# Optimization experiments

Hardware: AMD Instinct MI355X
Metric: run time of the kernel (lower is better)

Reference implementation:

```python
import jax, jax.numpy as jnp
import numpy as np

NUM_EXPERTS = 64
TOP_K = 2

def setup_inputs() -> dict:
    key = jax.random.key(0)
    k1, k2, k3, k4 = jax.random.split(key, 4)
    B, N, C, E = 4, 4096, 2048, NUM_EXPERTS
    x = jax.random.normal(k1, (B, N, C), dtype=jnp.float32)
    routing_context = jax.random.normal(k2, (B, C), dtype=jnp.float32)
    # Linear(C, E, bias=False) and Linear(C, C, bias=False), torch layout (out, in)
    gate_w = jax.random.normal(k3, (E, C), dtype=jnp.float32) * (1.0 / np.sqrt(C))
    ctx_w = jax.random.normal(k4, (C, C), dtype=jnp.float32) * (1.0 / np.sqrt(C))
    return {"x": x, "routing_context": routing_context, "gate_w": gate_w, "ctx_w": ctx_w}

def reference(x, routing_context, gate_w, ctx_w):
    B, N, C = x.shape
    T = B * N
    E = gate_w.shape[0]
    # context_proj(routing_context): (B,C) @ (C,C)^T -> broadcast over N
    ctx = routing_context @ ctx_w.T                      # (B, C)
    x_routing = (x + ctx[:, None, :]).reshape(T, C)      # (T, C)
    logits = x_routing @ gate_w.T                        # (T, E)
    top_vals, top_idx = jax.lax.top_k(logits, TOP_K)     # (T, K) each
    top_weights = jax.nn.softmax(top_vals, axis=-1)      # (T, K)
    probs = jax.nn.softmax(logits, axis=-1)              # (T, E)
    importance = probs.sum(axis=0) / T                   # (E,)
    # load: fraction of tokens that pick each expert in their top-k
    load = jnp.zeros((E,), dtype=probs.dtype).at[top_idx.reshape(-1)].add(1.0) / T
    aux_loss = E * (importance * load).sum()
    return top_idx, top_weights, aux_loss
```

## Files before the change

kernel.cpp:

```cpp
#include <hip/hip_runtime.h>
#include <math.h>

#define T_TOKENS 16384
#define C_DIM    2048
#define N_SEQ    4096
#define E_EXP    64
#define NSLICE   4
#define KSLICE   512
#define EPB      1024
#define GN       131072

typedef __attribute__((ext_vector_type(8))) short  short8;
typedef __attribute__((ext_vector_type(4))) float  floatx4;

__device__ __forceinline__ void splitv(float v, ushort& h, ushort& m, ushort& l) {
    unsigned u = __float_as_uint(v);
    h = (ushort)(u >> 16);
    float f1 = v - __uint_as_float(u & 0xffff0000u);
    unsigned u1 = __float_as_uint(f1);
    m = (ushort)(u1 >> 16);
    float f2 = f1 - __uint_as_float(u1 & 0xffff0000u);
    l = (ushort)(__float_as_uint(f2) >> 16);
}

__device__ __forceinline__ void splitpack8(const float4& a, const float4& b,
                                           short8& h, short8& m, short8& l) {
    ushort hh, mm, ll;
    splitv(a.x, hh, mm, ll); h[0] = hh; m[0] = mm; l[0] = ll;
    splitv(a.y, hh, mm, ll); h[1] = hh; m[1] = mm; l[1] = ll;
    splitv(a.z, hh, mm, ll); h[2] = hh; m[2] = mm; l[2] = ll;
    splitv(a.w, hh, mm, ll); h[3] = hh; m[3] = mm; l[3] = ll;
    splitv(b.x, hh, mm, ll); h[4] = hh; m[4] = mm; l[4] = ll;
    splitv(b.y, hh, mm, ll); h[5] = hh; m[5] = mm; l[5] = ll;
    splitv(b.z, hh, mm, ll); h[6] = hh; m[6] = mm; l[6] = ll;
    splitv(b.w, hh, mm, ll); h[7] = hh; m[7] = mm; l[7] = ll;
}

__device__ __forceinline__ void split3rne(float v, ushort& h, ushort& m, ushort& l) {
    unsigned u = __float_as_uint(v);
    unsigned r = (u + 0x7fffu + ((u >> 16) & 1u)) >> 16;
    h = (ushort)r;
    float e1 = v - __uint_as_float(r << 16);
    u = __float_as_uint(e1);
    r = (u + 0x7fffu + ((u >> 16) & 1u)) >> 16;
    m = (ushort)r;
    float e2 = e1 - __uint_as_float(r << 16);
    l = (ushort)(__float_as_uint(e2) >> 16);
}

__global__ __launch_bounds__(256, 2) void pre_kernel(
    const float* __restrict__ rc, const float* __restrict__ ctx_w,
    const float* __restrict__ gw, float* __restrict__ ctx_out,
    ushort* __restrict__ gsp)
{
    if (gsp != nullptr) {
        const int idx  = blockIdx.x * 256 + threadIdx.x;
        const int j    = idx & 7;
        const int e    = (idx >> 3) & 63;
        const int koct = idx >> 9;
        float g = gw[(size_t)e * C_DIM + koct * 8 + j];
        ushort h, m, l;
        split3rne(g, h, m, l);
        gsp[idx]          = h;
        gsp[GN + idx]     = m;
        gsp[2 * GN + idx] = l;
    }

    const int w    = threadIdx.x >> 6;
    const int lane = threadIdx.x & 63;
    const int j    = blockIdx.x * 4 + w;

    const float4* wr = (const float4*)(ctx_w + (size_t)j * C_DIM);
    const float4* r0 = (const float4*)(rc);
    const float4* r1 = (const float4*)(rc + C_DIM);
    const float4* r2 = (const float4*)(rc + 2 * C_DIM);
    const float4* r3 = (const float4*)(rc + 3 * C_DIM);

    float s0 = 0.f, s1 = 0.f, s2 = 0.f, s3 = 0.f;
#pragma unroll
    for (int it = 0; it < 8; ++it) {
        float4 a  = wr[it * 64 + lane];
        float4 c0 = r0[it * 64 + lane];
        float4 c1 = r1[it * 64 + lane];
        float4 c2 = r2[it * 64 + lane];
        float4 c3 = r3[it * 64 + lane];
        s0 += a.x * c0.x + a.y * c0.y + a.z * c0.z + a.w * c0.w;
        s1 += a.x * c1.x + a.y * c1.y + a.z * c1.z + a.w * c1.w;
        s2 += a.x * c2.x + a.y * c2.y + a.z * c2.z + a.w * c2.w;
        s3 += a.x * c3.x + a.y * c3.y + a.z * c3.z + a.w * c3.w;
    }
#pragma unroll
    for (int off = 32; off; off >>= 1) {
        s0 += __shfl_xor(s0, off, 64);
        s1 += __shfl_xor(s1, off, 64);
        s2 += __shfl_xor(s2, off, 64);
        s3 += __shfl_xor(s3, off, 64);
    }
    if (lane == 0) {
        ctx_out[j]             = s0;
        ctx_out[C_DIM + j]     = s1;
        ctx_out[2 * C_DIM + j] = s2;
        ctx_out[3 * C_DIM + j] = s3;
    }
}

__global__ __launch_bounds__(256, 2) void gemm_cl_kernel(
    const float* __restrict__ x, const ushort* __restrict__ gsp,
    const float* __restrict__ gw, const float* __restrict__ ctx,
    float* __restrict__ P, float* __restrict__ cl)
{
    if (blockIdx.x >= 128 * NSLICE) {
        const int lane = threadIdx.x & 63;
        const int pk   = (blockIdx.x - 128 * NSLICE) * 4 + (threadIdx.x >> 6);
        const int b    = pk >> 6;
        const int e    = pk & 63;
        const float4* wr = (const float4*)(gw + (size_t)e * C_DIM);
        const float4* cr = (const float4*)(ctx + (size_t)b * C_DIM);
        float s = 0.f;
#pragma unroll
        for (int it = 0; it < 8; ++it) {
            float4 a = wr[it * 64 + lane];
            float4 c = cr[it * 64 + lane];
            s += a.x * c.x + a.y * c.y + a.z * c.z + a.w * c.w;
        }
#pragma unroll
        for (int off = 32; off; off >>= 1) s += __shfl_xor(s, off, 64);
        if (lane == 0) cl[pk] = s;
        return;
    }

    const int tid   = threadIdx.x;
    const int wv    = tid >> 6;
    const int lane  = tid & 63;
    const int l15   = lane & 15;
    const int quad  = lane >> 4;
    const int tile  = blockIdx.x & 127;
    const int slice = blockIdx.x >> 7;
    const int tw    = tile * 128 + wv * 32;
    const int cbase = slice * KSLICE;

    floatx4 acc[2][4];
#pragma unroll
    for (int s = 0; s < 2; ++s)
#pragma unroll
        for (int nt = 0; nt < 4; ++nt) acc[s][nt] = (floatx4){0.f, 0.f, 0.f, 0.f};

    const float* xr0 = x + (size_t)(tw + l15) * C_DIM + cbase + quad * 8;
    const float* xr1 = xr0 + (size_t)16 * C_DIM;
    const ushort* bb = gsp + ((size_t)((cbase >> 3) + quad) * 64 + l15) * 8;

    const int NKS = KSLICE / 32;

    float4 a00 = *(const float4*)(xr0);
    float4 a01 = *(const float4*)(xr0 + 4);
    float4 a10 = *(const float4*)(xr1);
    float4 a11 = *(const float4*)(xr1 + 4);

#pragma unroll 2
    for (int ks = 0; ks < NKS; ++ks) {
        const int nk = (ks + 1 < NKS) ? (ks + 1) : 0;
        float4 n00 = *(const float4*)(xr0 + nk * 32);
        float4 n01 = *(const float4*)(xr0 + nk * 32 + 4);
        float4 n10 = *(const float4*)(xr1 + nk * 32);
        float4 n11 = *(const float4*)(xr1 + nk * 32 + 4);

        const ushort* bks = bb + (size_t)ks * 4 * 64 * 8;
        short8 bh[4], bm[4], bl[4];
#pragma unroll
        for (int nt = 0; nt < 4; ++nt) {
            const ushort* bp_ = bks + (size_t)(16 * nt) * 8;
            bh[nt] = *(const short8*)(bp_);
            bm[nt] = *(const short8*)(bp_ + GN);
            bl[nt] = *(const short8*)(bp_ + 2 * (size_t)GN);
        }

        short8 ah0, am0, al0, ah1, am1, al1;
        splitpack8(a00, a01, ah0, am0, al0);
        splitpack8(a10, a11, ah1, am1, al1);

#pragma unroll
        for (int nt = 0; nt < 4; ++nt) {
            acc[0][nt] = __builtin_amdgcn_mfma_f32_16x16x32_bf16(ah0, bh[nt], acc[0][nt], 0, 0, 0);
            acc[0][nt] = __builtin_amdgcn_mfma_f32_16x16x32_bf16(ah0, bm[nt], acc[0][nt], 0, 0, 0);
            acc[0][nt] = __builtin_amdgcn_mfma_f32_16x16x32_bf16(am0, bh[nt], acc[0][nt], 0, 0, 0);
            acc[0][nt] = __builtin_amdgcn_mfma_f32_16x16x32_bf16(ah0, bl[nt], acc[0][nt], 0, 0, 0);
            acc[0][nt] = __builtin_amdgcn_mfma_f32_16x16x32_bf16(al0, bh[nt], acc[0][nt], 0, 0, 0);
            acc[0][nt] = __builtin_amdgcn_mfma_f32_16x16x32_bf16(am0, bm[nt], acc[0][nt], 0, 0, 0);
            acc[1][nt] = __builtin_amdgcn_mfma_f32_16x16x32_bf16(ah1, bh[nt], acc[1][nt], 0, 0, 0);
            acc[1][nt] = __builtin_amdgcn_mfma_f32_16x16x32_bf16(ah1, bm[nt], acc[1][nt], 0, 0, 0);
            acc[1][nt] = __builtin_amdgcn_mfma_f32_16x16x32_bf16(am1, bh[nt], acc[1][nt], 0, 0, 0);
            acc[1][nt] = __builtin_amdgcn_mfma_f32_16x16x32_bf16(ah1, bl[nt], acc[1][nt], 0, 0, 0);
            acc[1][nt] = __builtin_amdgcn_mfma_f32_16x16x32_bf16(al1, bh[nt], acc[1][nt], 0, 0, 0);
            acc[1][nt] = __builtin_amdgcn_mfma_f32_16x16x32_bf16(am1, bm[nt], acc[1][nt], 0, 0, 0);
        }

        a00 = n00; a01 = n01; a10 = n10; a11 = n11;
    }

    float* Ps = P + ((size_t)slice * T_TOKENS + tw) * E_EXP;
#pragma unroll
    for (int s = 0; s < 2; ++s)
#pragma unroll
        for (int nt = 0; nt < 4; ++nt)
#pragma unroll
            for (int r = 0; r < 4; ++r)
                Ps[(size_t)(s * 16 + quad * 4 + r) * E_EXP + 16 * nt + l15] =
                    acc[s][nt][r];
}

__global__ __launch_bounds__(256) void epilogue_kernel(
    const float* __restrict__ P, const float* __restrict__ cl,
    float* __restrict__ out, float* __restrict__ bp)
{
    __shared__ float red[4][128];

    const int tid  = threadIdx.x;
    const int wv   = tid >> 6;
    const int lane = tid & 63;
    const int t0   = blockIdx.x * (T_TOKENS / EPB);
    const float clv = cl[(t0 >> 12) * 64 + lane];

    float imp_acc = 0.f, cnt_acc = 0.f;

    for (int tt = 0; tt < 4; ++tt) {
        const int t = t0 + wv * 4 + tt;
        float v = clv;
#pragma unroll
        for (int s = 0; s < NSLICE; ++s)
            v += P[((size_t)s * T_TOKENS + t) * E_EXP + lane];

        const float p = expf(v);
        float v1 = v;  int i1 = lane;
        float v2 = -INFINITY; int i2 = 0x7fffffff;
        float s = p;
#pragma unroll
        for (int off = 32; off; off >>= 1) {
            float ov1 = __shfl_xor(v1, off, 64);
            int   oi1 = __shfl_xor(i1, off, 64);
            float ov2 = __shfl_xor(v2, off, 64);
            int   oi2 = __shfl_xor(i2, off, 64);
            s += __shfl_xor(s, off, 64);
            const bool aw = (ov1 < v1) || (ov1 == v1 && i1 < oi1);
            const float lv = aw ? ov1 : v1;  const int li = aw ? oi1 : i1;
            const float wv2 = aw ? v2 : ov2; const int wi = aw ? i2 : oi2;
            if (!aw) { v1 = ov1; i1 = oi1; }
            const bool sw = (wv2 < lv) || (wv2 == lv && li < wi);
            v2 = sw ? lv : wv2; i2 = sw ? li : wi;
        }

        imp_acc += p / s;
        if (lane == i1 || lane == i2) cnt_acc += 1.f;

        if (lane == 0) {
            const float e2 = expf(v2 - v1);
            out[2 * t]     = (float)i1;
            out[2 * t + 1] = (float)i2;
            out[2 * T_TOKENS + 2 * t]     = 1.f / (1.f + e2);
            out[2 * T_TOKENS + 2 * t + 1] = e2 / (1.f + e2);
        }
    }

    red[wv][lane]      = imp_acc;
    red[wv][64 + lane] = cnt_acc;
    __syncthreads();
    if (tid < 128) {
        float s = red[0][tid] + red[1][tid] + red[2][tid] + red[3][tid];
        bp[(size_t)blockIdx.x * 128 + tid] = s;
    }
}

__global__ __launch_bounds__(1024) void aux_kernel(
    const float* __restrict__ bp, int nb, float* __restrict__ out_aux)
{
    __shared__ float4 red[32][32];
    const int tid = threadIdx.x;
    const int c4  = tid & 31;
    const int grp = tid >> 5;

    const float4* bp4 = (const float4*)bp;
    float4 s = make_float4(0.f, 0.f, 0.f, 0.f);
    for (int r = grp; r < nb; r += 32) {
        float4 v = bp4[(size_t)r * 32 + c4];
        s.x += v.x; s.y += v.y; s.z += v.z; s.w += v.w;
    }
    red[grp][c4] = s;
    __syncthreads();

    if (tid < 32) {
        float4 t = make_float4(0.f, 0.f, 0.f, 0.f);
#pragma unroll
        for (int g = 0; g < 32; ++g) {
            float4 v = red[g][tid];
            t.x += v.x; t.y += v.y; t.z += v.z; t.w += v.w;
        }
        red[0][tid] = t;
    }
    __syncthreads();

    if (tid < 16) {
        float4 a = red[0][tid];
        float4 b = red[0][tid + 16];
        float v = a.x * b.x + a.y * b.y + a.z * b.z + a.w * b.w;
#pragma unroll
        for (int off = 8; off; off >>= 1) v += __shfl_xor(v, off, 64);
        if (tid == 0)
            out_aux[0] = (float)E_EXP * v / ((float)T_TOKENS * (float)T_TOKENS);
    }
}

#define TM    64
#define FKC   64
#define FLSTR 68
__global__ __launch_bounds__(256) void router_fused_kernel(
    const float* __restrict__ x, const float* __restrict__ gate_w,
    const float* __restrict__ ctx, float* __restrict__ out,
    float* __restrict__ bp)
{
    __shared__ float xs[TM][FLSTR];
    __shared__ float gs[E_EXP][FLSTR];
    __shared__ float ls[TM][FLSTR];
    __shared__ float red[4][128];

    const int tid = threadIdx.x;
    const int eg  = tid & 15;
    const int tg  = tid >> 4;
    const int t0  = blockIdx.x * TM;
    const int b   = t0 / N_SEQ;
    const int sr  = tid >> 4;
    const int scg = tid & 15;
    const float* ctx_row = ctx + (size_t)b * C_DIM;

    float4 acc[4][4];
#pragma unroll
    for (int i = 0; i < 4; ++i)
#pragma unroll
        for (int j = 0; j < 4; ++j) acc[i][j] = make_float4(0.f, 0.f, 0.f, 0.f);

    float4 px[4], pg[4], pc;
    auto prefetch = [&](int kc) {
        const int c0 = kc * FKC + scg * 4;
        pc = *(const float4*)(ctx_row + c0);
#pragma unroll
        for (int i = 0; i < 4; ++i) {
            px[i] = *(const float4*)(x + (size_t)(t0 + sr + 16 * i) * C_DIM + c0);
            pg[i] = *(const float4*)(gate_w + (size_t)(sr + 16 * i) * C_DIM + c0);
        }
    };

    prefetch(0);
    const int NCHUNK = C_DIM / FKC;
    for (int kc = 0; kc < NCHUNK; ++kc) {
        __syncthreads();
#pragma unroll
        for (int i = 0; i < 4; ++i) {
            float4 v = px[i];
            v.x += pc.x; v.y += pc.y; v.z += pc.z; v.w += pc.w;
            *(float4*)&xs[sr + 16 * i][scg * 4] = v;
            *(float4*)&gs[sr + 16 * i][scg * 4] = pg[i];
        }
        __syncthreads();
        if (kc + 1 < NCHUNK) prefetch(kc + 1);
#pragma unroll
        for (int cc = 0; cc < FKC; cc += 4) {
            float4 xv[4], gv[4];
#pragma unroll
            for (int i = 0; i < 4; ++i) xv[i] = *(const float4*)&xs[tg + 16 * i][cc];
#pragma unroll
            for (int j = 0; j < 4; ++j) gv[j] = *(const float4*)&gs[eg + 16 * j][cc];
#pragma unroll
            for (int i = 0; i < 4; ++i)
#pragma unroll
                for (int j = 0; j < 4; ++j) {
                    acc[i][j].x = fmaf(xv[i].x, gv[j].x, acc[i][j].x);
                    acc[i][j].y = fmaf(xv[i].y, gv[j].y, acc[i][j].y);
                    acc[i][j].z = fmaf(xv[i].z, gv[j].z, acc[i][j].z);
                    acc[i][j].w = fmaf(xv[i].w, gv[j].w, acc[i][j].w);
                }
        }
    }

    __syncthreads();
#pragma unroll
    for (int i = 0; i < 4; ++i)
#pragma unroll
        for (int j = 0; j < 4; ++j)
            ls[tg + 16 * i][eg + 16 * j] =
                (acc[i][j].x + acc[i][j].y) + (acc[i][j].z + acc[i][j].w);
    __syncthreads();

    const int wv   = tid >> 6;
    const int lane = tid & 63;
    float imp_acc = 0.f, cnt_acc = 0.f;

    for (int tt = 0; tt < 16; ++tt) {
        const int tokL = wv * 16 + tt;
        const float v = ls[tokL][lane];
        const float p = expf(v);
        float v1 = v;  int i1 = lane;
        float v2 = -INFINITY; int i2 = 0x7fffffff;
        float s = p;
#pragma unroll
        for (int off = 32; off; off >>= 1) {
            float ov1 = __shfl_xor(v1, off, 64);
            int   oi1 = __shfl_xor(i1, off, 64);
            float ov2 = __shfl_xor(v2, off, 64);
            int   oi2 = __shfl_xor(i2, off, 64);
            s += __shfl_xor(s, off, 64);
            const bool aw = (ov1 < v1) || (ov1 == v1 && i1 < oi1);
            const float lv = aw ? ov1 : v1;  const int li = aw ? oi1 : i1;
            const float wv2 = aw ? v2 : ov2; const int wi = aw ? i2 : oi2;
            if (!aw) { v1 = ov1; i1 = oi1; }
            const bool sw = (wv2 < lv) || (wv2 == lv && li < wi);
            v2 = sw ? lv : wv2; i2 = sw ? li : wi;
        }
        imp_acc += p / s;
        if (lane == i1 || lane == i2) cnt_acc += 1.f;
        if (lane == 0) {
            const int t = t0 + tokL;
            const float e2 = expf(v2 - v1);
            out[2 * t]     = (float)i1;
            out[2 * t + 1] = (float)i2;
            out[2 * T_TOKENS + 2 * t]     = 1.f / (1.f + e2);
            out[2 * T_TOKENS + 2 * t + 1] = e2 / (1.f + e2);
        }
    }

    red[wv][lane]      = imp_acc;
    red[wv][64 + lane] = cnt_acc;
    __syncthreads();
    if (tid < 128) {
        float s = red[0][tid] + red[1][tid] + red[2][tid] + red[3][tid];
        bp[(size_t)blockIdx.x * 128 + tid] = s;
    }
}

extern "C" void kernel_launch(void* const* d_in, const int* in_sizes, int n_in,
                              void* d_out, int out_size, void* d_ws, size_t ws_size,
                              hipStream_t stream)
{
    (void)in_sizes; (void)n_in; (void)out_size;
    const float* x      = (const float*)d_in[0];
    const float* rc     = (const float*)d_in[1];
    const float* gate_w = (const float*)d_in[2];
    const float* ctx_w  = (const float*)d_in[3];
    float* out = (float*)d_out;

    float*  ctx = (float*)d_ws;
    float*  cl  = ctx + 8192;
    float*  bp  = cl + 256;
    float*  P   = bp + (size_t)EPB * 128;
    ushort* gsp = (ushort*)(P + (size_t)NSLICE * T_TOKENS * E_EXP);

    const size_t need =
        (8192 + 256 + (size_t)EPB * 128 + (size_t)NSLICE * T_TOKENS * E_EXP)
            * sizeof(float)
        + (size_t)3 * GN * sizeof(ushort);

    if (ws_size >= need) {
        pre_kernel<<<512, 256, 0, stream>>>(rc, ctx_w, gate_w, ctx, gsp);
        gemm_cl_kernel<<<128 * NSLICE + 64, 256, 0, stream>>>(x, gsp, gate_w, ctx, P, cl);
        epilogue_kernel<<<EPB, 256, 0, stream>>>(P, cl, out, bp);
        aux_kernel<<<1, 1024, 0, stream>>>(bp, EPB, out + 2 * 2 * T_TOKENS);
    } else {
        pre_kernel<<<512, 256, 0, stream>>>(rc, ctx_w, gate_w, ctx, nullptr);
        router_fused_kernel<<<256, 256, 0, stream>>>(x, gate_w, ctx, out, bp);
        aux_kernel<<<1, 1024, 0, stream>>>(bp, 256, out + 2 * 2 * T_TOKENS);
    }
}
```

Baseline: 246.2 us.

## Overlap context projection with the main GEMM and move cl into its own kernel

The context-projection GEMV (ctx_w @ routing_context) moves out of the pre-kernel and into extra blocks of the main bf16-split GEMM kernel, so its 16 MB ctx_w read runs alongside the x GEMM. The pre-stage now only does the gate weight split. The ctx-by-gate_w dot products (cl) go into a small separate kernel launched after the GEMM, because they depend on ctx. This adds one kernel launch, and the extra ctx blocks compete with the GEMM tiles for bandwidth and compute units.

```diff
diff --git a/kernel.cpp b/kernel.cpp
--- a/kernel.cpp
+++ b/kernel.cpp
@@ -48,28 +48,10 @@
     l = (ushort)(__float_as_uint(e2) >> 16);
 }
 
-__global__ __launch_bounds__(256, 2) void pre_kernel(
-    const float* __restrict__ rc, const float* __restrict__ ctx_w,
-    const float* __restrict__ gw, float* __restrict__ ctx_out,
-    ushort* __restrict__ gsp)
-{
-    if (gsp != nullptr) {
-        const int idx  = blockIdx.x * 256 + threadIdx.x;
-        const int j    = idx & 7;
-        const int e    = (idx >> 3) & 63;
-        const int koct = idx >> 9;
-        float g = gw[(size_t)e * C_DIM + koct * 8 + j];
-        ushort h, m, l;
-        split3rne(g, h, m, l);
-        gsp[idx]          = h;
-        gsp[GN + idx]     = m;
-        gsp[2 * GN + idx] = l;
-    }
-
-    const int w    = threadIdx.x >> 6;
-    const int lane = threadIdx.x & 63;
-    const int j    = blockIdx.x * 4 + w;
-
+__device__ __forceinline__ void ctx_body(
+    int j, int lane, const float* __restrict__ rc,
+    const float* __restrict__ ctx_w, float* __restrict__ ctx_out)
+{
     const float4* wr = (const float4*)(ctx_w + (size_t)j * C_DIM);
     const float4* r0 = (const float4*)(rc);
     const float4* r1 = (const float4*)(rc + C_DIM);
@@ -104,28 +86,30 @@
     }
 }
 
-__global__ __launch_bounds__(256, 2) void gemm_cl_kernel(
+__global__ __launch_bounds__(256) void split_kernel(
+    const float* __restrict__ gw, ushort* __restrict__ gsp)
+{
+    const int idx  = blockIdx.x * 256 + threadIdx.x;
+    const int j    = idx & 7;
+    const int e    = (idx >> 3) & 63;
+    const int koct = idx >> 9;
+    float g = gw[(size_t)e * C_DIM + koct * 8 + j];
+    ushort h, m, l;
+    split3rne(g, h, m, l);
+    gsp[idx]          = h;
+    gsp[GN + idx]     = m;
+    gsp[2 * GN + idx] = l;
+}
+
+__global__ __launch_bounds__(256, 2) void gemm_ctx_kernel(
     const float* __restrict__ x, const ushort* __restrict__ gsp,
-    const float* __restrict__ gw, const float* __restrict__ ctx,
-    float* __restrict__ P, float* __restrict__ cl)
+    const float* __restrict__ rc, const float* __restrict__ ctx_w,
+    float* __restrict__ ctx_out, float* __restrict__ P)
 {
     if (blockIdx.x >= 128 * NSLICE) {
         const int lane = threadIdx.x & 63;
-        const int pk   = (blockIdx.x - 128 * NSLICE) * 4 + (threadIdx.x >> 6);
-        const int b    = pk >> 6;
-        const int e    = pk & 63;
-        const float4* wr = (const float4*)(gw + (size_t)e * C_DIM);
-        const float4* cr = (const float4*)(ctx + (size_t)b * C_DIM);
-        float s = 0.f;
-#pragma unroll
-        for (int it = 0; it < 8; ++it) {
-            float4 a = wr[it * 64 + lane];
-            float4 c = cr[it * 64 + lane];
-            s += a.x * c.x + a.y * c.y + a.z * c.z + a.w * c.w;
-        }
-#pragma unroll
-        for (int off = 32; off; off >>= 1) s += __shfl_xor(s, off, 64);
-        if (lane == 0) cl[pk] = s;
+        const int j = (blockIdx.x - 128 * NSLICE) * 4 + (threadIdx.x >> 6);
+        ctx_body(j, lane, rc, ctx_w, ctx_out);
         return;
     }
 
@@ -208,6 +192,28 @@
                     acc[s][nt][r];
 }
 
+__global__ __launch_bounds__(256) void cl_kernel(
+    const float* __restrict__ gw, const float* __restrict__ ctx,
+    float* __restrict__ cl)
+{
+    const int lane = threadIdx.x & 63;
+    const int pk   = blockIdx.x * 4 + (threadIdx.x >> 6);
+    const int b    = pk >> 6;
+    const int e    = pk & 63;
+    const float4* wr = (const float4*)(gw + (size_t)e * C_DIM);
+    const float4* cr = (const float4*)(ctx + (size_t)b * C_DIM);
+    float s = 0.f;
+#pragma unroll
+    for (int it = 0; it < 8; ++it) {
+        float4 a = wr[it * 64 + lane];
+        float4 c = cr[it * 64 + lane];
+        s += a.x * c.x + a.y * c.y + a.z * c.z + a.w * c.w;
+    }
+#pragma unroll
+    for (int off = 32; off; off >>= 1) s += __shfl_xor(s, off, 64);
+    if (lane == 0) cl[pk] = s;
+}
+
 __global__ __launch_bounds__(256) void epilogue_kernel(
     const float* __restrict__ P, const float* __restrict__ cl,
     float* __restrict__ out, float* __restrict__ bp)
@@ -308,6 +314,15 @@
     }
 }
 
+__global__ __launch_bounds__(256) void ctx_only_kernel(
+    const float* __restrict__ rc, const float* __restrict__ ctx_w,
+    float* __restrict__ ctx_out)
+{
+    const int lane = threadIdx.x & 63;
+    const int j    = blockIdx.x * 4 + (threadIdx.x >> 6);
+    ctx_body(j, lane, rc, ctx_w, ctx_out);
+}
+
 #define TM    64
 #define FKC   64
 #define FLSTR 68
@@ -457,12 +472,14 @@
         + (size_t)3 * GN * sizeof(ushort);
 
     if (ws_size >= need) {
-        pre_kernel<<<512, 256, 0, stream>>>(rc, ctx_w, gate_w, ctx, gsp);
-        gemm_cl_kernel<<<128 * NSLICE + 64, 256, 0, stream>>>(x, gsp, gate_w, ctx, P, cl);
+        split_kernel<<<512, 256, 0, stream>>>(gate_w, gsp);
+        gemm_ctx_kernel<<<128 * NSLICE + 512, 256, 0, stream>>>(
+            x, gsp, rc, ctx_w, ctx, P);
+        cl_kernel<<<64, 256, 0, stream>>>(gate_w, ctx, cl);
         epilogue_kernel<<<EPB, 256, 0, stream>>>(P, cl, out, bp);
         aux_kernel<<<1, 1024, 0, stream>>>(bp, EPB, out + 2 * 2 * T_TOKENS);
     } else {
-        pre_kernel<<<512, 256, 0, stream>>>(rc, ctx_w, gate_w, ctx, nullptr);
+        ctx_only_kernel<<<512, 256, 0, stream>>>(rc, ctx_w, ctx);
         router_fused_kernel<<<256, 256, 0, stream>>>(x, gate_w, ctx, out, bp);
         aux_kernel<<<1, 1024, 0, stream>>>(bp, 256, out + 2 * 2 * T_TOKENS);
     }
```

New measurement: 245.8 us. Within noise of the previous version (-0.1%).

## Fuse full-K MFMA gate GEMM with top-k epilogue, drop split-K partials

Applied to the files above, without the earlier changes.

Replaces the split-K GEMM plus separate epilogue with one kernel where each 2-wave block computes full-K logits for 32 tokens and does top-2, softmax and per-block reductions in registers via lane shuffles. This eliminates writing and rereading the 4-slice partial logit buffer and one kernel launch. The context-logit bias moves to a small standalone kernel. The tradeoff is fewer, longer-running waves with lower occupancy, which may reduce latency hiding on the dominant x stream.

```diff
diff --git a/kernel.cpp b/kernel.cpp
--- a/kernel.cpp
+++ b/kernel.cpp
@@ -5,10 +5,8 @@
 #define C_DIM    2048
 #define N_SEQ    4096
 #define E_EXP    64
-#define NSLICE   4
-#define KSLICE   512
-#define EPB      1024
 #define GN       131072
+#define FBLK     512
 
 typedef __attribute__((ext_vector_type(8))) short  short8;
 typedef __attribute__((ext_vector_type(4))) float  floatx4;
@@ -48,7 +46,45 @@
     l = (ushort)(__float_as_uint(e2) >> 16);
 }
 
-__global__ __launch_bounds__(256, 2) void pre_kernel(
+__device__ __forceinline__ void ctx_body(
+    int j, int lane, const float* __restrict__ rc,
+    const float* __restrict__ ctx_w, float* __restrict__ ctx_out)
+{
+    const float4* wr = (const float4*)(ctx_w + (size_t)j * C_DIM);
+    const float4* r0 = (const float4*)(rc);
+    const float4* r1 = (const float4*)(rc + C_DIM);
+    const float4* r2 = (const float4*)(rc + 2 * C_DIM);
+    const float4* r3 = (const float4*)(rc + 3 * C_DIM);
+
+    float s0 = 0.f, s1 = 0.f, s2 = 0.f, s3 = 0.f;
+#pragma unroll
+    for (int it = 0; it < 8; ++it) {
+        float4 a  = wr[it * 64 + lane];
+        float4 c0 = r0[it * 64 + lane];
+        float4 c1 = r1[it * 64 + lane];
+        float4 c2 = r2[it * 64 + lane];
+        float4 c3 = r3[it * 64 + lane];
+        s0 += a.x * c0.x + a.y * c0.y + a.z * c0.z + a.w * c0.w;
+        s1 += a.x * c1.x + a.y * c1.y + a.z * c1.z + a.w * c1.w;
+        s2 += a.x * c2.x + a.y * c2.y + a.z * c2.z + a.w * c2.w;
+        s3 += a.x * c3.x + a.y * c3.y + a.z * c3.z + a.w * c3.w;
+    }
+#pragma unroll
+    for (int off = 32; off; off >>= 1) {
+        s0 += __shfl_xor(s0, off, 64);
+        s1 += __shfl_xor(s1, off, 64);
+        s2 += __shfl_xor(s2, off, 64);
+        s3 += __shfl_xor(s3, off, 64);
+    }
+    if (lane == 0) {
+        ctx_out[j]             = s0;
+        ctx_out[C_DIM + j]     = s1;
+        ctx_out[2 * C_DIM + j] = s2;
+        ctx_out[3 * C_DIM + j] = s3;
+    }
+}
+
+__global__ __launch_bounds__(256) void pre_kernel(
     const float* __restrict__ rc, const float* __restrict__ ctx_w,
     const float* __restrict__ gw, float* __restrict__ ctx_out,
     ushort* __restrict__ gsp)
@@ -65,106 +101,66 @@
         gsp[GN + idx]     = m;
         gsp[2 * GN + idx] = l;
     }
-
-    const int w    = threadIdx.x >> 6;
     const int lane = threadIdx.x & 63;
-    const int j    = blockIdx.x * 4 + w;
-
-    const float4* wr = (const float4*)(ctx_w + (size_t)j * C_DIM);
-    const float4* r0 = (const float4*)(rc);
-    const float4* r1 = (const float4*)(rc + C_DIM);
-    const float4* r2 = (const float4*)(rc + 2 * C_DIM);
-    const float4* r3 = (const float4*)(rc + 3 * C_DIM);
-
-    float s0 = 0.f, s1 = 0.f, s2 = 0.f, s3 = 0.f;
+    const int j    = blockIdx.x * 4 + (threadIdx.x >> 6);
+    ctx_body(j, lane, rc, ctx_w, ctx_out);
+}
+
+__global__ __launch_bounds__(256) void cl_kernel(
+    const float* __restrict__ gw, const float* __restrict__ ctx,
+    float* __restrict__ cl)
+{
+    const int lane = threadIdx.x & 63;
+    const int pk   = blockIdx.x * 4 + (threadIdx.x >> 6);
+    const int b    = pk >> 6;
+    const int e    = pk & 63;
+    const float4* wr = (const float4*)(gw + (size_t)e * C_DIM);
+    const float4* cr = (const float4*)(ctx + (size_t)b * C_DIM);
+    float s = 0.f;
 #pragma unroll
     for (int it = 0; it < 8; ++it) {
-        float4 a  = wr[it * 64 + lane];
-        float4 c0 = r0[it * 64 + lane];
-        float4 c1 = r1[it * 64 + lane];
-        float4 c2 = r2[it * 64 + lane];
-        float4 c3 = r3[it * 64 + lane];
-        s0 += a.x * c0.x + a.y * c0.y + a.z * c0.z + a.w * c0.w;
-        s1 += a.x * c1.x + a.y * c1.y + a.z * c1.z + a.w * c1.w;
-        s2 += a.x * c2.x + a.y * c2.y + a.z * c2.z + a.w * c2.w;
-        s3 += a.x * c3.x + a.y * c3.y + a.z * c3.z + a.w * c3.w;
-    }
-#pragma unroll
-    for (int off = 32; off; off >>= 1) {
-        s0 += __shfl_xor(s0, off, 64);
-        s1 += __shfl_xor(s1, off, 64);
-        s2 += __shfl_xor(s2, off, 64);
-        s3 += __shfl_xor(s3, off, 64);
-    }
-    if (lane == 0) {
-        ctx_out[j]             = s0;
-        ctx_out[C_DIM + j]     = s1;
-        ctx_out[2 * C_DIM + j] = s2;
-        ctx_out[3 * C_DIM + j] = s3;
-    }
-}
-
-__global__ __launch_bounds__(256, 2) void gemm_cl_kernel(
+        float4 a = wr[it * 64 + lane];
+        float4 c = cr[it * 64 + lane];
+        s += a.x * c.x + a.y * c.y + a.z * c.z + a.w * c.w;
+    }
+#pragma unroll
+    for (int off = 32; off; off >>= 1) s += __shfl_xor(s, off, 64);
+    if (lane == 0) cl[pk] = s;
+}
+
+__global__ __launch_bounds__(128, 1) void fused_kernel(
     const float* __restrict__ x, const ushort* __restrict__ gsp,
-    const float* __restrict__ gw, const float* __restrict__ ctx,
-    float* __restrict__ P, float* __restrict__ cl)
-{
-    if (blockIdx.x >= 128 * NSLICE) {
-        const int lane = threadIdx.x & 63;
-        const int pk   = (blockIdx.x - 128 * NSLICE) * 4 + (threadIdx.x >> 6);
-        const int b    = pk >> 6;
-        const int e    = pk & 63;
-        const float4* wr = (const float4*)(gw + (size_t)e * C_DIM);
-        const float4* cr = (const float4*)(ctx + (size_t)b * C_DIM);
-        float s = 0.f;
-#pragma unroll
-        for (int it = 0; it < 8; ++it) {
-            float4 a = wr[it * 64 + lane];
-            float4 c = cr[it * 64 + lane];
-            s += a.x * c.x + a.y * c.y + a.z * c.z + a.w * c.w;
-        }
-#pragma unroll
-        for (int off = 32; off; off >>= 1) s += __shfl_xor(s, off, 64);
-        if (lane == 0) cl[pk] = s;
-        return;
-    }
-
-    const int tid   = threadIdx.x;
-    const int wv    = tid >> 6;
-    const int lane  = tid & 63;
-    const int l15   = lane & 15;
-    const int quad  = lane >> 4;
-    const int tile  = blockIdx.x & 127;
-    const int slice = blockIdx.x >> 7;
-    const int tw    = tile * 128 + wv * 32;
-    const int cbase = slice * KSLICE;
-
-    floatx4 acc[2][4];
-#pragma unroll
-    for (int s = 0; s < 2; ++s)
-#pragma unroll
-        for (int nt = 0; nt < 4; ++nt) acc[s][nt] = (floatx4){0.f, 0.f, 0.f, 0.f};
-
-    const float* xr0 = x + (size_t)(tw + l15) * C_DIM + cbase + quad * 8;
-    const float* xr1 = xr0 + (size_t)16 * C_DIM;
-    const ushort* bb = gsp + ((size_t)((cbase >> 3) + quad) * 64 + l15) * 8;
-
-    const int NKS = KSLICE / 32;
-
-    float4 a00 = *(const float4*)(xr0);
-    float4 a01 = *(const float4*)(xr0 + 4);
-    float4 a10 = *(const float4*)(xr1);
-    float4 a11 = *(const float4*)(xr1 + 4);
+    const float* __restrict__ cl, float* __restrict__ out,
+    float* __restrict__ bp)
+{
+    __shared__ float red[2][128];
+
+    const int tid  = threadIdx.x;
+    const int wv   = tid >> 6;
+    const int lane = tid & 63;
+    const int l15  = lane & 15;
+    const int quad = lane >> 4;
+    const int t0   = blockIdx.x * 32;
+    const int b    = t0 >> 12;
+
+    floatx4 acc[4];
+#pragma unroll
+    for (int nt = 0; nt < 4; ++nt) acc[nt] = (floatx4){0.f, 0.f, 0.f, 0.f};
+
+    const float* xr = x + (size_t)(t0 + wv * 16 + l15) * C_DIM + quad * 8;
+
+    float4 a00 = *(const float4*)(xr);
+    float4 a01 = *(const float4*)(xr + 4);
+    float4 n00 = *(const float4*)(xr + 32);
+    float4 n01 = *(const float4*)(xr + 36);
 
 #pragma unroll 2
-    for (int ks = 0; ks < NKS; ++ks) {
-        const int nk = (ks + 1 < NKS) ? (ks + 1) : 0;
-        float4 n00 = *(const float4*)(xr0 + nk * 32);
-        float4 n01 = *(const float4*)(xr0 + nk * 32 + 4);
-        float4 n10 = *(const float4*)(xr1 + nk * 32);
-        float4 n11 = *(const float4*)(xr1 + nk * 32 + 4);
-
-        const ushort* bks = bb + (size_t)ks * 4 * 64 * 8;
+    for (int ks = 0; ks < 64; ++ks) {
+        const int fk = (ks + 2 < 64) ? ks + 2 : 0;
+        float4 f00 = *(const float4*)(xr + fk * 32);
+        float4 f01 = *(const float4*)(xr + fk * 32 + 4);
+
+        const ushort* bks = gsp + ((size_t)(ks * 4 + quad) * 64 + l15) * 8;
         short8 bh[4], bm[4], bl[4];
 #pragma unroll
         for (int nt = 0; nt < 4; ++nt) {
@@ -174,61 +170,225 @@
             bl[nt] = *(const short8*)(bp_ + 2 * (size_t)GN);
         }
 
-        short8 ah0, am0, al0, ah1, am1, al1;
-        splitpack8(a00, a01, ah0, am0, al0);
-        splitpack8(a10, a11, ah1, am1, al1);
+        short8 ah, am, al;
+        splitpack8(a00, a01, ah, am, al);
 
 #pragma unroll
         for (int nt = 0; nt < 4; ++nt) {
-            acc[0][nt] = __builtin_amdgcn_mfma_f32_16x16x32_bf16(ah0, bh[nt], acc[0][nt], 0, 0, 0);
-            acc[0][nt] = __builtin_amdgcn_mfma_f32_16x16x32_bf16(ah0, bm[nt], acc[0][nt], 0, 0, 0);
-            acc[0][nt] = __builtin_amdgcn_mfma_f32_16x16x32_bf16(am0, bh[nt], acc[0][nt], 0, 0, 0);
-            acc[0][nt] = __builtin_amdgcn_mfma_f32_16x16x32_bf16(ah0, bl[nt], acc[0][nt], 0, 0, 0);
-            acc[0][nt] = __builtin_amdgcn_mfma_f32_16x16x32_bf16(al0, bh[nt], acc[0][nt], 0, 0, 0);
-            acc[0][nt] = __builtin_amdgcn_mfma_f32_16x16x32_bf16(am0, bm[nt], acc[0][nt], 0, 0, 0);
-            acc[1][nt] = __builtin_amdgcn_mfma_f32_16x16x32_bf16(ah1, bh[nt], acc[1][nt], 0, 0, 0);
-            acc[1][nt] = __builtin_amdgcn_mfma_f32_16x16x32_bf16(ah1, bm[nt], acc[1][nt], 0, 0, 0);
-            acc[1][nt] = __builtin_amdgcn_mfma_f32_16x16x32_bf16(am1, bh[nt], acc[1][nt], 0, 0, 0);
-            acc[1][nt] = __builtin_amdgcn_mfma_f32_16x16x32_bf16(ah1, bl[nt], acc[1][nt], 0, 0, 0);
-            acc[1][nt] = __builtin_amdgcn_mfma_f32_16x16x32_bf16(al1, bh[nt], acc[1][nt], 0, 0, 0);
-            acc[1][nt] = __builtin_amdgcn_mfma_f32_16x16x32_bf16(am1, bm[nt], acc[1][nt], 0, 0, 0);
-        }
-
-        a00 = n00; a01 = n01; a10 = n10; a11 = n11;
-    }
-
-    float* Ps = P + ((size_t)slice * T_TOKENS + tw) * E_EXP;
-#pragma unroll
-    for (int s = 0; s < 2; ++s)
-#pragma unroll
-        for (int nt = 0; nt < 4; ++nt)
-#pragma unroll
-            for (int r = 0; r < 4; ++r)
-                Ps[(size_t)(s * 16 + quad * 4 + r) * E_EXP + 16 * nt + l15] =
-                    acc[s][nt][r];
-}
-
-__global__ __launch_bounds__(256) void epilogue_kernel(
-    const float* __restrict__ P, const float* __restrict__ cl,
-    float* __restrict__ out, float* __restrict__ bp)
-{
+            acc[nt] = __builtin_amdgcn_mfma_f32_16x16x32_bf16(ah, bh[nt], acc[nt], 0, 0, 0);
+            acc[nt] = __builtin_amdgcn_mfma_f32_16x16x32_bf16(ah, bm[nt], acc[nt], 0, 0, 0);
+            acc[nt] = __builtin_amdgcn_mfma_f32_16x16x32_bf16(am, bh[nt], acc[nt], 0, 0, 0);
+            acc[nt] = __builtin_amdgcn_mfma_f32_16x16x32_bf16(ah, bl[nt], acc[nt], 0, 0, 0);
+            acc[nt] = __builtin_amdgcn_mfma_f32_16x16x32_bf16(al, bh[nt], acc[nt], 0, 0, 0);
+            acc[nt] = __builtin_amdgcn_mfma_f32_16x16x32_bf16(am, bm[nt], acc[nt], 0, 0, 0);
+        }
+
+        a00 = n00; a01 = n01; n00 = f00; n01 = f01;
+    }
+
+    float clv[4];
+#pragma unroll
+    for (int nt = 0; nt < 4; ++nt) clv[nt] = cl[b * 64 + 16 * nt + l15];
+
+    float imp4[4] = {0.f, 0.f, 0.f, 0.f};
+    float cnt4[4] = {0.f, 0.f, 0.f, 0.f};
+
+#pragma unroll
+    for (int r = 0; r < 4; ++r) {
+        const int t = t0 + wv * 16 + quad * 4 + r;
+        float v[4], p[4];
+#pragma unroll
+        for (int nt = 0; nt < 4; ++nt) {
+            v[nt] = acc[nt][r] + clv[nt];
+            p[nt] = expf(v[nt]);
+        }
+        float s = (p[0] + p[1]) + (p[2] + p[3]);
+
+        float v1 = v[0];      int i1 = l15;
+        float v2 = -INFINITY; int i2 = 0x7fffffff;
+#pragma unroll
+        for (int k = 1; k < 4; ++k) {
+            const int e = 16 * k + l15;
+            if (v[k] > v1) { v2 = v1; i2 = i1; v1 = v[k]; i1 = e; }
+            else if (v[k] > v2 || (v[k] == v2 && e < i2)) { v2 = v[k]; i2 = e; }
+        }
+
+#pragma unroll
+        for (int off = 8; off; off >>= 1) {
+            float ov1 = __shfl_xor(v1, off, 64);
+            int   oi1 = __shfl_xor(i1, off, 64);
+            float ov2 = __shfl_xor(v2, off, 64);
+            int   oi2 = __shfl_xor(i2, off, 64);
+            s += __shfl_xor(s, off, 64);
+            const bool aw = (ov1 < v1) || (ov1 == v1 && i1 < oi1);
+            const float lv = aw ? ov1 : v1;  const int li = aw ? oi1 : i1;
+            const float wv2 = aw ? v2 : ov2; const int wi = aw ? i2 : oi2;
+            if (!aw) { v1 = ov1; i1 = oi1; }
+            const bool sw = (wv2 < lv) || (wv2 == lv && li < wi);
+            v2 = sw ? lv : wv2; i2 = sw ? li : wi;
+        }
+
+#pragma unroll
+        for (int nt = 0; nt < 4; ++nt) {
+            const int e = 16 * nt + l15;
+            imp4[nt] += p[nt] / s;
+            cnt4[nt] += ((e == i1) ? 1.f : 0.f) + ((e == i2) ? 1.f : 0.f);
+        }
+
+        if (l15 == 0) {
+            const float e2 = expf(v2 - v1);
+            out[2 * t]     = (float)i1;
+            out[2 * t + 1] = (float)i2;
+            out[2 * T_TOKENS + 2 * t]     = 1.f / (1.f + e2);
+            out[2 * T_TOKENS + 2 * t + 1] = e2 / (1.f + e2);
+        }
+    }
+
+#pragma unroll
+    for (int nt = 0; nt < 4; ++nt) {
+        imp4[nt] += __shfl_xor(imp4[nt], 16, 64);
+        imp4[nt] += __shfl_xor(imp4[nt], 32, 64);
+        cnt4[nt] += __shfl_xor(cnt4[nt], 16, 64);
+        cnt4[nt] += __shfl_xor(cnt4[nt], 32, 64);
+    }
+    if (quad == 0) {
+#pragma unroll
+        for (int nt = 0; nt < 4; ++nt) {
+            red[wv][16 * nt + l15]      = imp4[nt];
+            red[wv][64 + 16 * nt + l15] = cnt4[nt];
+        }
+    }
+    __syncthreads();
+    if (tid < 128)
+        bp[(size_t)blockIdx.x * 128 + tid] = red[0][tid] + red[1][tid];
+}
+
+__global__ __launch_bounds__(1024) void aux_kernel(
+    const float* __restrict__ bp, int nb, float* __restrict__ out_aux)
+{
+    __shared__ float4 red[32][32];
+    const int tid = threadIdx.x;
+    const int c4  = tid & 31;
+    const int grp = tid >> 5;
+
+    const float4* bp4 = (const float4*)bp;
+    float4 s = make_float4(0.f, 0.f, 0.f, 0.f);
+    for (int r = grp; r < nb; r += 32) {
+        float4 v = bp4[(size_t)r * 32 + c4];
+        s.x += v.x; s.y += v.y; s.z += v.z; s.w += v.w;
+    }
+    red[grp][c4] = s;
+    __syncthreads();
+
+    if (tid < 32) {
+        float4 t = make_float4(0.f, 0.f, 0.f, 0.f);
+#pragma unroll
+        for (int g = 0; g < 32; ++g) {
+            float4 v = red[g][tid];
+            t.x += v.x; t.y += v.y; t.z += v.z; t.w += v.w;
+        }
+        red[0][tid] = t;
+    }
+    __syncthreads();
+
+    if (tid < 16) {
+        float4 a = red[0][tid];
+        float4 b = red[0][tid + 16];
+        float v = a.x * b.x + a.y * b.y + a.z * b.z + a.w * b.w;
+#pragma unroll
+        for (int off = 8; off; off >>= 1) v += __shfl_xor(v, off, 64);
+        if (tid == 0)
+            out_aux[0] = (float)E_EXP * v / ((float)T_TOKENS * (float)T_TOKENS);
+    }
+}
+
+#define TM    64
+#define FKC   64
+#define FLSTR 68
+__global__ __launch_bounds__(256) void router_fused_kernel(
+    const float* __restrict__ x, const float* __restrict__ gate_w,
+    const float* __restrict__ ctx, float* __restrict__ out,
+    float* __restrict__ bp)
+{
+    __shared__ float xs[TM][FLSTR];
+    __shared__ float gs[E_EXP][FLSTR];
+    __shared__ float ls[TM][FLSTR];
     __shared__ float red[4][128];
 
-    const int tid  = threadIdx.x;
+    const int tid = threadIdx.x;
+    const int eg  = tid & 15;
+    const int tg  = tid >> 4;
+    const int t0  = blockIdx.x * TM;
+    const int b   = t0 / N_SEQ;
+    const int sr  = tid >> 4;
+    const int scg = tid & 15;
+    const float* ctx_row = ctx + (size_t)b * C_DIM;
+
+    float4 acc[4][4];
+#pragma unroll
+    for (int i = 0; i < 4; ++i)
+#pragma unroll
+        for (int j = 0; j < 4; ++j) acc[i][j] = make_float4(0.f, 0.f, 0.f, 0.f);
+
+    float4 px[4], pg[4], pc;
+    auto prefetch = [&](int kc) {
+        const int c0 = kc * FKC + scg * 4;
+        pc = *(const float4*)(ctx_row + c0);
+#pragma unroll
+        for (int i = 0; i < 4; ++i) {
+            px[i] = *(const float4*)(x + (size_t)(t0 + sr + 16 * i) * C_DIM + c0);
+            pg[i] = *(const float4*)(gate_w + (size_t)(sr + 16 * i) * C_DIM + c0);
+        }
+    };
+
+    prefetch(0);
+    const int NCHUNK = C_DIM / FKC;
+    for (int kc = 0; kc < NCHUNK; ++kc) {
+        __syncthreads();
+#pragma unroll
+        for (int i = 0; i < 4; ++i) {
+            float4 v = px[i];
+            v.x += pc.x; v.y += pc.y; v.z += pc.z; v.w += pc.w;
+            *(float4*)&xs[sr + 16 * i][scg * 4] = v;
+            *(float4*)&gs[sr + 16 * i][scg * 4] = pg[i];
+        }
+        __syncthreads();
+        if (kc + 1 < NCHUNK) prefetch(kc + 1);
+#pragma unroll
+        for (int cc = 0; cc < FKC; cc += 4) {
+            float4 xv[4], gv[4];
+#pragma unroll
+            for (int i = 0; i < 4; ++i) xv[i] = *(const float4*)&xs[tg + 16 * i][cc];
+#pragma unroll
+            for (int j = 0; j < 4; ++j) gv[j] = *(const float4*)&gs[eg + 16 * j][cc];
+#pragma unroll
+            for (int i = 0; i < 4; ++i)
+#pragma unroll
+                for (int j = 0; j < 4; ++j) {
+                    acc[i][j].x = fmaf(xv[i].x, gv[j].x, acc[i][j].x);
+                    acc[i][j].y = fmaf(xv[i].y, gv[j].y, acc[i][j].y);
+                    acc[i][j].z = fmaf(xv[i].z, gv[j].z, acc[i][j].z);
+                    acc[i][j].w = fmaf(xv[i].w, gv[j].w, acc[i][j].w);
+                }
+        }
+    }
+
+    __syncthreads();
+#pragma unroll
+    for (int i = 0; i < 4; ++i)
+#pragma unroll
+        for (int j = 0; j < 4; ++j)
+            ls[tg + 16 * i][eg + 16 * j] =
+                (acc[i][j].x + acc[i][j].y) + (acc[i][j].z + acc[i][j].w);
+    __syncthreads();
+
     const int wv   = tid >> 6;
     const int lane = tid & 63;
-    const int t0   = blockIdx.x * (T_TOKENS / EPB);
-    const float clv = cl[(t0 >> 12) * 64 + lane];
-
     float imp_acc = 0.f, cnt_acc = 0.f;
 
-    for (int tt = 0; tt < 4; ++tt) {
-        const int t = t0 + wv * 4 + tt;
-        float v = clv;
-#pragma unroll
-        for (int s = 0; s < NSLICE; ++s)
-            v += P[((size_t)s * T_TOKENS + t) * E_EXP + lane];
-
+    for (int tt = 0; tt < 16; ++tt) {
+        const int tokL = wv * 16 + tt;
+        const float v = ls[tokL][lane];
         const float p = expf(v);
         float v1 = v;  int i1 = lane;
         float v2 = -INFINITY; int i2 = 0x7fffffff;
@@ -247,172 +407,6 @@
             const bool sw = (wv2 < lv) || (wv2 == lv && li < wi);
             v2 = sw ? lv : wv2; i2 = sw ? li : wi;
         }
-
-        imp_acc += p / s;
-        if (lane == i1 || lane == i2) cnt_acc += 1.f;
-
-        if (lane == 0) {
-            const float e2 = expf(v2 - v1);
-            out[2 * t]     = (float)i1;
-            out[2 * t + 1] = (float)i2;
-            out[2 * T_TOKENS + 2 * t]     = 1.f / (1.f + e2);
-            out[2 * T_TOKENS + 2 * t + 1] = e2 / (1.f + e2);
-        }
-    }
-
-    red[wv][lane]      = imp_acc;
-    red[wv][64 + lane] = cnt_acc;
-    __syncthreads();
-    if (tid < 128) {
-        float s = red[0][tid] + red[1][tid] + red[2][tid] + red[3][tid];
-        bp[(size_t)blockIdx.x * 128 + tid] = s;
-    }
-}
-
-__global__ __launch_bounds__(1024) void aux_kernel(
-    const float* __restrict__ bp, int nb, float* __restrict__ out_aux)
-{
-    __shared__ float4 red[32][32];
-    const int tid = threadIdx.x;
-    const int c4  = tid & 31;
-    const int grp = tid >> 5;
-
-    const float4* bp4 = (const float4*)bp;
-    float4 s = make_float4(0.f, 0.f, 0.f, 0.f);
-    for (int r = grp; r < nb; r += 32) {
-        float4 v = bp4[(size_t)r * 32 + c4];
-        s.x += v.x; s.y += v.y; s.z += v.z; s.w += v.w;
-    }
-    red[grp][c4] = s;
-    __syncthreads();
-
-    if (tid < 32) {
-        float4 t = make_float4(0.f, 0.f, 0.f, 0.f);
-#pragma unroll
-        for (int g = 0; g < 32; ++g) {
-            float4 v = red[g][tid];
-            t.x += v.x; t.y += v.y; t.z += v.z; t.w += v.w;
-        }
-        red[0][tid] = t;
-    }
-    __syncthreads();
-
-    if (tid < 16) {
-        float4 a = red[0][tid];
-        float4 b = red[0][tid + 16];
-        float v = a.x * b.x + a.y * b.y + a.z * b.z + a.w * b.w;
-#pragma unroll
-        for (int off = 8; off; off >>= 1) v += __shfl_xor(v, off, 64);
-        if (tid == 0)
-            out_aux[0] = (float)E_EXP * v / ((float)T_TOKENS * (float)T_TOKENS);
-    }
-}
-
-#define TM    64
-#define FKC   64
-#define FLSTR 68
-__global__ __launch_bounds__(256) void router_fused_kernel(
-    const float* __restrict__ x, const float* __restrict__ gate_w,
-    const float* __restrict__ ctx, float* __restrict__ out,
-    float* __restrict__ bp)
-{
-    __shared__ float xs[TM][FLSTR];
-    __shared__ float gs[E_EXP][FLSTR];
-    __shared__ float ls[TM][FLSTR];
-    __shared__ float red[4][128];
-
-    const int tid = threadIdx.x;
-    const int eg  = tid & 15;
-    const int tg  = tid >> 4;
-    const int t0  = blockIdx.x * TM;
-    const int b   = t0 / N_SEQ;
-    const int sr  = tid >> 4;
-    const int scg = tid & 15;
-    const float* ctx_row = ctx + (size_t)b * C_DIM;
-
-    float4 acc[4][4];
-#pragma unroll
-    for (int i = 0; i < 4; ++i)
-#pragma unroll
-        for (int j = 0; j < 4; ++j) acc[i][j] = make_float4(0.f, 0.f, 0.f, 0.f);
-
-    float4 px[4], pg[4], pc;
-    auto prefetch = [&](int kc) {
-        const int c0 = kc * FKC + scg * 4;
-        pc = *(const float4*)(ctx_row + c0);
-#pragma unroll
-        for (int i = 0; i < 4; ++i) {
-            px[i] = *(const float4*)(x + (size_t)(t0 + sr + 16 * i) * C_DIM + c0);
-            pg[i] = *(const float4*)(gate_w + (size_t)(sr + 16 * i) * C_DIM + c0);
-        }
-    };
-
-    prefetch(0);
-    const int NCHUNK = C_DIM / FKC;
-    for (int kc = 0; kc < NCHUNK; ++kc) {
-        __syncthreads();
-#pragma unroll
-        for (int i = 0; i < 4; ++i) {
-            float4 v = px[i];
-            v.x += pc.x; v.y += pc.y; v.z += pc.z; v.w += pc.w;
-            *(float4*)&xs[sr + 16 * i][scg * 4] = v;
-            *(float4*)&gs[sr + 16 * i][scg * 4] = pg[i];
-        }
-        __syncthreads();
-        if (kc + 1 < NCHUNK) prefetch(kc + 1);
-#pragma unroll
-        for (int cc = 0; cc < FKC; cc += 4) {
-            float4 xv[4], gv[4];
-#pragma unroll
-            for (int i = 0; i < 4; ++i) xv[i] = *(const float4*)&xs[tg + 16 * i][cc];
-#pragma unroll
-            for (int j = 0; j < 4; ++j) gv[j] = *(const float4*)&gs[eg + 16 * j][cc];
-#pragma unroll
-            for (int i = 0; i < 4; ++i)
-#pragma unroll
-                for (int j = 0; j < 4; ++j) {
-                    acc[i][j].x = fmaf(xv[i].x, gv[j].x, acc[i][j].x);
-                    acc[i][j].y = fmaf(xv[i].y, gv[j].y, acc[i][j].y);
-                    acc[i][j].z = fmaf(xv[i].z, gv[j].z, acc[i][j].z);
-                    acc[i][j].w = fmaf(xv[i].w, gv[j].w, acc[i][j].w);
-                }
-        }
-    }
-
-    __syncthreads();
-#pragma unroll
-    for (int i = 0; i < 4; ++i)
-#pragma unroll
-        for (int j = 0; j < 4; ++j)
-            ls[tg + 16 * i][eg + 16 * j] =
-                (acc[i][j].x + acc[i][j].y) + (acc[i][j].z + acc[i][j].w);
-    __syncthreads();
-
-    const int wv   = tid >> 6;
-    const int lane = tid & 63;
-    float imp_acc = 0.f, cnt_acc = 0.f;
-
-    for (int tt = 0; tt < 16; ++tt) {
-        const int tokL = wv * 16 + tt;
-        const float v = ls[tokL][lane];
-        const float p = expf(v);
-        float v1 = v;  int i1 = lane;
-        float v2 = -INFINITY; int i2 = 0x7fffffff;
-        float s = p;
-#pragma unroll
-        for (int off = 32; off; off >>= 1) {
-            float ov1 = __shfl_xor(v1, off, 64);
-            int   oi1 = __shfl_xor(i1, off, 64);
-            float ov2 = __shfl_xor(v2, off, 64);
-            int   oi2 = __shfl_xor(i2, off, 64);
-            s += __shfl_xor(s, off, 64);
-            const bool aw = (ov1 < v1) || (ov1 == v1 && i1 < oi1);
-            const float lv = aw ? ov1 : v1;  const int li = aw ? oi1 : i1;
-            const float wv2 = aw ? v2 : ov2; const int wi = aw ? i2 : oi2;
-            if (!aw) { v1 = ov1; i1 = oi1; }
-            const bool sw = (wv2 < lv) || (wv2 == lv && li < wi);
-            v2 = sw ? lv : wv2; i2 = sw ? li : wi;
-        }
         imp_acc += p / s;
         if (lane == i1 || lane == i2) cnt_acc += 1.f;
         if (lane == 0) {
@@ -448,19 +442,17 @@
     float*  ctx = (float*)d_ws;
     float*  cl  = ctx + 8192;
     float*  bp  = cl + 256;
-    float*  P   = bp + (size_t)EPB * 128;
-    ushort* gsp = (ushort*)(P + (size_t)NSLICE * T_TOKENS * E_EXP);
+    ushort* gsp = (ushort*)(bp + (size_t)FBLK * 128);
 
     const size_t need =
-        (8192 + 256 + (size_t)EPB * 128 + (size_t)NSLICE * T_TOKENS * E_EXP)
-            * sizeof(float)
+        (8192 + 256 + (size_t)FBLK * 128) * sizeof(float)
         + (size_t)3 * GN * sizeof(ushort);
 
     if (ws_size >= need) {
         pre_kernel<<<512, 256, 0, stream>>>(rc, ctx_w, gate_w, ctx, gsp);
-        gemm_cl_kernel<<<128 * NSLICE + 64, 256, 0, stream>>>(x, gsp, gate_w, ctx, P, cl);
-        epilogue_kernel<<<EPB, 256, 0, stream>>>(P, cl, out, bp);
-        aux_kernel<<<1, 1024, 0, stream>>>(bp, EPB, out + 2 * 2 * T_TOKENS);
+        cl_kernel<<<64, 256, 0, stream>>>(gate_w, ctx, cl);
+        fused_kernel<<<FBLK, 128, 0, stream>>>(x, gsp, cl, out, bp);
+        aux_kernel<<<1, 1024, 0, stream>>>(bp, FBLK, out + 2 * 2 * T_TOKENS);
     } else {
         pre_kernel<<<512, 256, 0, stream>>>(rc, ctx_w, gate_w, ctx, nullptr);
         router_fused_kernel<<<256, 256, 0, stream>>>(x, gate_w, ctx, out, bp);
```

After: 254.0 us. +3.2%, slower.
